# Kernel tuning notes

Measured on AMD Instinct MI355X. Metric: run time of the kernel, lower is better.

## Reference

```python
import jax, jax.numpy as jnp
import numpy as np

SA_LAMBDA = 1.0
IC_LAMBDA = 1.0
EPS = 1e-12  # torch F.normalize eps


def setup_inputs() -> dict:
    key = jax.random.key(0)
    k1, k2, k3, k4 = jax.random.split(key, 4)
    TF = jax.random.normal(k1, (16, 512, 32, 32), dtype=jnp.float32)
    SF = jax.random.normal(k2, (16, 512, 32, 32), dtype=jnp.float32)
    t_out = jax.random.normal(k3, (16, 21, 128, 128), dtype=jnp.float32)
    s_out = jax.random.normal(k4, (16, 21, 128, 128), dtype=jnp.float32)
    return {"TF": TF, "SF": SF, "t_out": t_out, "s_out": s_out}


def _l2_normalize_last(A):
    # matches torch.nn.functional.normalize(x, dim=2): x / max(||x||, eps)
    n = jnp.linalg.norm(A, axis=-1, keepdims=True)
    return A / jnp.maximum(n, EPS)


def _channel_weighted_spatial_gram(F4):
    # Algebraic fusion of einsum('bij,bki->bijk') + einsum('bijk,bi->bjk'):
    # ATT[b,m,n] = sum_c F[b,c,m] * F[b,c,n] * Fc[b,c]
    b, c, h, w = F4.shape
    Fc = jnp.sum(jnp.abs(F4), axis=(2, 3))          # [b, c]
    Fm = F4.reshape(b, c, h * w)                     # [b, c, M]
    A = jnp.einsum('bcm,bc,bcn->bmn', Fm, Fc, Fm)    # [b, M, M]
    return _l2_normalize_last(A)


def _normalized_channel_gram(L):
    # ICC[b,i,j] = sum_m L[b,i,m] * L[b,j,m], then L2-normalize along last dim
    G = jnp.einsum('bim,bjm->bij', L, L)
    return _l2_normalize_last(G)


def reference(TF, SF, t_out, s_out):
    b, c, h, w = TF.shape
    M = h * w
    ATT_T = _channel_weighted_spatial_gram(TF)
    ATT_S = _channel_weighted_spatial_gram(SF)
    diff = ATT_S - ATT_T
    SA_loss = SA_LAMBDA * jnp.sum(diff * diff) / (b * M ** 2)

    bb, cc, hh, ww = s_out.shape
    s_logit = s_out.reshape(bb, cc, hh * ww)
    t_logit = t_out.reshape(bb, cc, hh * ww)
    G_diff = _normalized_channel_gram(s_logit) - _normalized_channel_gram(t_logit)
    ic_loss = IC_LAMBDA * jnp.sum(G_diff * G_diff) / (cc * bb)

    return (s_out, ic_loss, SA_loss)
```

## Files before the change

kernel.cpp:

```cpp
#include <hip/hip_runtime.h>
#include <hip/hip_bf16.h>
#include <cstdint>
#include <cstddef>

typedef __bf16 bf16x8 __attribute__((ext_vector_type(8)));
typedef float f32x4 __attribute__((ext_vector_type(4)));

__device__ __forceinline__ void gload_lds16(const void* g, void* l) {
  __builtin_amdgcn_global_load_lds((const __attribute__((address_space(1))) void*)g,
                                   (__attribute__((address_space(3))) void*)l, 16, 0, 0);
}
__device__ __forceinline__ unsigned short f2bf(float x) {
  return __builtin_bit_cast(unsigned short, __float2bfloat16(x));
}
#define S_BARRIER asm volatile("s_barrier" ::: "memory")
#define WAIT_VM(N) asm volatile("s_waitcnt vmcnt(" #N ")" ::: "memory")

__global__ void fc_kernel(const float* __restrict__ TF, const float* __restrict__ SF,
                          float* __restrict__ sqrtFc) {
  int wv = threadIdx.x >> 6, lane = threadIdx.x & 63;
  int row = blockIdx.x * 4 + wv;
  const float* X = (row < 8192) ? TF : SF;
  const float* p = X + (size_t)(row & 8191) * 1024;
  float s = 0.f;
#pragma unroll
  for (int it = 0; it < 4; ++it) {
    float4 v = *reinterpret_cast<const float4*>(p + (size_t)(it * 64 + lane) * 4);
    s += fabsf(v.x) + fabsf(v.y) + fabsf(v.z) + fabsf(v.w);
  }
#pragma unroll
  for (int m = 32; m; m >>= 1) s += __shfl_xor(s, m);
  if (lane == 0) sqrtFc[row] = sqrtf(s);
}

__global__ void __launch_bounds__(256) wprep2_kernel(const float* __restrict__ TF,
                                                     const float* __restrict__ SF,
                                                     const float* __restrict__ sqrtFc,
                                                     __hip_bfloat16* __restrict__ Wt,
                                                     __hip_bfloat16* __restrict__ Ws) {
  __shared__ float lds[64][65];
  __shared__ float scale[64];
  int z = blockIdx.z;
  int t = z >> 4, b = z & 15;
  int m0 = blockIdx.x * 64, c0 = blockIdx.y * 64;
  const float* Xg = (t ? SF : TF) + (size_t)b * 524288;
  __hip_bfloat16* Wg = (t ? Ws : Wt) + (size_t)b * 524288;
  int tid = threadIdx.x;
  if (tid < 64) scale[tid] = sqrtFc[t * 8192 + b * 512 + c0 + tid];
#pragma unroll
  for (int i = 0; i < 4; ++i) {
    int v = i * 256 + tid;
    int r = v >> 4, q = v & 15;
    *reinterpret_cast<float4*>(&lds[r][q * 4]) =
        *reinterpret_cast<const float4*>(Xg + (size_t)(c0 + r) * 1024 + m0 + q * 4);
  }
  __syncthreads();
#pragma unroll
  for (int jj = 0; jj < 2; ++jj) {
    int m = jj * 32 + (tid >> 3), oct = tid & 7;
    union { unsigned short h[8]; uint4 u; } pk;
#pragma unroll
    for (int k = 0; k < 8; ++k) {
      int c = oct * 8 + k;
      pk.h[k] = f2bf(lds[c][m] * scale[c]);
    }
    *reinterpret_cast<uint4*>(Wg + (size_t)(m0 + m) * 512 + c0 + oct * 8) = pk.u;
  }
}

__global__ void __launch_bounds__(512, 4) syrk_fused_kernel(
    const __hip_bfloat16* __restrict__ Wt, const __hip_bfloat16* __restrict__ Ws,
    float* __restrict__ nT, float* __restrict__ nS, float* __restrict__ cross) {
  __shared__ __hip_bfloat16 AL[2][128 * 64];
  __shared__ __hip_bfloat16 BL[2][128 * 64];
  int bid = blockIdx.x;
  int j = (bid & 7) * 72 + (bid >> 3);
  int b = j / 36, pair = j % 36;
  int bx = pair, tm = 0;
  while (bx >= 8 - tm) { bx -= 8 - tm; ++tm; }
  int tn = tm + bx;
  bool diag = (tm == tn);
  const __hip_bfloat16* WTb = Wt + (size_t)b * 524288;
  const __hip_bfloat16* WSb = Ws + (size_t)b * 524288;
  const __hip_bfloat16* ATp = WTb + (size_t)tm * 65536;
  const __hip_bfloat16* ASp = WSb + (size_t)tm * 65536;
  const __hip_bfloat16* BTp = WTb + (size_t)tn * 65536;
  const __hip_bfloat16* BSp = WSb + (size_t)tn * 65536;

  const int tid = threadIdx.x;
  const int lane = tid & 63, wv = tid >> 6;
  const int wr = wv >> 1, wc = wv & 1;
  const int g = lane >> 4, c0 = lane & 15, cx = c0 & 7;

  int offs[2], dst[2];
#pragma unroll
  for (int i = 0; i < 2; ++i) {
    int ci = i * 512 + tid;
    int row = ci >> 3, slot = ci & 7;
    offs[i] = row * 512 + (slot ^ (row & 7)) * 8;
    dst[i] = (i * 512 + wv * 64) * 8;
  }

  f32x4 accT[2][4], accS[2][4];
#pragma unroll
  for (int mi = 0; mi < 2; ++mi)
#pragma unroll
    for (int ni = 0; ni < 4; ++ni) {
      accT[mi][ni] = (f32x4){0.f, 0.f, 0.f, 0.f};
      accS[mi][ni] = (f32x4){0.f, 0.f, 0.f, 0.f};
    }

  auto stage = [&](int s, int buf) {
    int kt = (s & 7) * 64;
    const __hip_bfloat16* Ab = (s < 8) ? ATp : ASp;
    const __hip_bfloat16* Bb = (s < 8) ? BTp : BSp;
#pragma unroll
    for (int i = 0; i < 2; ++i) {
      gload_lds16(Ab + offs[i] + kt, &AL[buf][dst[i]]);
      gload_lds16(Bb + offs[i] + kt, &BL[buf][dst[i]]);
    }
  };

  stage(0, 0);
#pragma unroll
  for (int s = 0; s < 16; ++s) {
    int buf = s & 1;
    if (s < 15) {
      stage(s + 1, buf ^ 1);
      WAIT_VM(4);
    } else {
      WAIT_VM(0);
    }
    S_BARRIER;
    const __hip_bfloat16* Ab = AL[buf];
    const __hip_bfloat16* Bb = BL[buf];
#pragma unroll
    for (int kk = 0; kk < 2; ++kk) {
      int ck = ((kk * 4 + g) ^ cx) * 8;
      bf16x8 av[2], bv[4];
#pragma unroll
      for (int mi = 0; mi < 2; ++mi)
        av[mi] = *reinterpret_cast<const bf16x8*>(Ab + (wr * 32 + mi * 16 + c0) * 64 + ck);
#pragma unroll
      for (int ni = 0; ni < 4; ++ni)
        bv[ni] = *reinterpret_cast<const bf16x8*>(Bb + (wc * 64 + ni * 16 + c0) * 64 + ck);
      if (s < 8) {
#pragma unroll
        for (int mi = 0; mi < 2; ++mi)
#pragma unroll
          for (int ni = 0; ni < 4; ++ni)
            accT[mi][ni] = __builtin_amdgcn_mfma_f32_16x16x32_bf16(av[mi], bv[ni], accT[mi][ni], 0, 0, 0);
      } else {
#pragma unroll
        for (int mi = 0; mi < 2; ++mi)
#pragma unroll
          for (int ni = 0; ni < 4; ++ni)
            accS[mi][ni] = __builtin_amdgcn_mfma_f32_16x16x32_bf16(av[mi], bv[ni], accS[mi][ni], 0, 0, 0);
      }
    }
    if (s < 15) S_BARRIER;
  }

  float* pT = nT + (size_t)b * 1024;
  float* pS = nS + (size_t)b * 1024;
  float* pC = cross + (size_t)b * 1024;
#pragma unroll
  for (int mi = 0; mi < 2; ++mi)
#pragma unroll
    for (int r = 0; r < 4; ++r) {
      float sT = 0.f, sS = 0.f, sC = 0.f;
#pragma unroll
      for (int ni = 0; ni < 4; ++ni) {
        float tv = accT[mi][ni][r], sv = accS[mi][ni][r];
        sT += tv * tv; sS += sv * sv; sC += tv * sv;
      }
#pragma unroll
      for (int msk = 1; msk < 16; msk <<= 1) {
        sT += __shfl_xor(sT, msk); sS += __shfl_xor(sS, msk); sC += __shfl_xor(sC, msk);
      }
      if (c0 == 0) {
        int m = tm * 128 + wr * 32 + mi * 16 + g * 4 + r;
        atomicAdd(pT + m, sT); atomicAdd(pS + m, sS); atomicAdd(pC + m, sC);
      }
    }
  if (!diag) {
#pragma unroll
    for (int ni = 0; ni < 4; ++ni) {
      float sT = 0.f, sS = 0.f, sC = 0.f;
#pragma unroll
      for (int mi = 0; mi < 2; ++mi)
#pragma unroll
        for (int r = 0; r < 4; ++r) {
          float tv = accT[mi][ni][r], sv = accS[mi][ni][r];
          sT += tv * tv; sS += sv * sv; sC += tv * sv;
        }
      sT += __shfl_xor(sT, 16); sS += __shfl_xor(sS, 16); sC += __shfl_xor(sC, 16);
      sT += __shfl_xor(sT, 32); sS += __shfl_xor(sS, 32); sC += __shfl_xor(sC, 32);
      if (g == 0) {
        int n = tn * 128 + wc * 64 + ni * 16 + c0;
        atomicAdd(pT + n, sT); atomicAdd(pS + n, sS); atomicAdd(pC + n, sC);
      }
    }
  }
}

__global__ void __launch_bounds__(256) icgram3_kernel(const float* __restrict__ t_out,
                                                      const float* __restrict__ s_out,
                                                      float* __restrict__ G,
                                                      float* __restrict__ outcpy) {
  __shared__ float lds[21 * 516];
  int chunk = blockIdx.x;
  int z = blockIdx.y;
  int t = z >> 4, bb = z & 15;
  const float* L = (t ? s_out : t_out) + (size_t)bb * 344064 + (size_t)chunk * 512;
  float* O = outcpy + (size_t)bb * 344064 + (size_t)chunk * 512;
  int tid = threadIdx.x;
  for (int idx = tid; idx < 21 * 128; idx += 256) {
    int r = idx >> 7, c = idx & 127;
    float4 v = *reinterpret_cast<const float4*>(L + (size_t)r * 16384 + c * 4);
    if (t) *reinterpret_cast<float4*>(O + (size_t)r * 16384 + c * 4) = v;
    *reinterpret_cast<float4*>(&lds[r * 516 + c * 4]) = v;
  }
  __syncthreads();
  int wv = tid >> 6, lane = tid & 63;
  float* Gz = G + (size_t)z * 441;
  for (int sp = wv; sp < 66; sp += 4) {
    int pp = sp, gi = 0;
    while (pp >= 11 - gi) { pp -= 11 - gi; ++gi; }
    int gj = gi + pp;
    int i0 = 2 * gi, j0 = 2 * gj;
    bool i1v = (i0 + 1 < 21), j1v = (j0 + 1 < 21);
    const float4* Ri0 = reinterpret_cast<const float4*>(&lds[i0 * 516]);
    const float4* Ri1 = reinterpret_cast<const float4*>(&lds[(i1v ? i0 + 1 : i0) * 516]);
    const float4* Rj0 = reinterpret_cast<const float4*>(&lds[j0 * 516]);
    const float4* Rj1 = reinterpret_cast<const float4*>(&lds[(j1v ? j0 + 1 : j0) * 516]);
    float4 a00 = Ri0[lane], a01 = Ri0[lane + 64];
    float4 a10 = Ri1[lane], a11 = Ri1[lane + 64];
    float4 b00 = Rj0[lane], b01 = Rj0[lane + 64];
    float4 b10 = Rj1[lane], b11 = Rj1[lane + 64];
    float s00 = a00.x * b00.x + a00.y * b00.y + a00.z * b00.z + a00.w * b00.w
              + a01.x * b01.x + a01.y * b01.y + a01.z * b01.z + a01.w * b01.w;
    float s01 = a00.x * b10.x + a00.y * b10.y + a00.z * b10.z + a00.w * b10.w
              + a01.x * b11.x + a01.y * b11.y + a01.z * b11.z + a01.w * b11.w;
    float s10 = a10.x * b00.x + a10.y * b00.y + a10.z * b00.z + a10.w * b00.w
              + a11.x * b01.x + a11.y * b01.y + a11.z * b01.z + a11.w * b01.w;
    float s11 = a10.x * b10.x + a10.y * b10.y + a10.z * b10.z + a10.w * b10.w
              + a11.x * b11.x + a11.y * b11.y + a11.z * b11.z + a11.w * b11.w;
    s00 += __shfl_xor(s00, 1); s00 += __shfl_xor(s00, 2);
    s01 += __shfl_xor(s01, 1); s01 += __shfl_xor(s01, 2);
    s10 += __shfl_xor(s10, 1); s10 += __shfl_xor(s10, 2);
    s11 += __shfl_xor(s11, 1); s11 += __shfl_xor(s11, 2);
    int q = lane & 3;
    float sq = (q == 0) ? s00 : (q == 1) ? s01 : (q == 2) ? s10 : s11;
    sq += __shfl_xor(sq, 4); sq += __shfl_xor(sq, 8);
    sq += __shfl_xor(sq, 16); sq += __shfl_xor(sq, 32);
    if (lane < 4) {
      bool ok = (lane == 0) || (lane == 1 && j1v) ||
                (lane == 2 && i1v && gi != gj) || (lane == 3 && i1v && j1v);
      int ii = (lane >> 1) ? i0 + 1 : i0;
      int jj = (lane & 1) ? j0 + 1 : j0;
      if (ok) atomicAdd(&Gz[ii * 21 + jj], sq);
    }
  }
}

__global__ void finalize_kernel(const float* __restrict__ G, const float* __restrict__ nT,
                                const float* __restrict__ nS, const float* __restrict__ cross,
                                float* __restrict__ out2) {
  __shared__ float red[16];
  int tid = threadIdx.x;
  float sa = 0.f;
#pragma unroll
  for (int it = 0; it < 4; ++it) {
    int i4 = it * 1024 + tid;
    float4 a = reinterpret_cast<const float4*>(nT)[i4];
    float4 s4 = reinterpret_cast<const float4*>(nS)[i4];
    float4 c4 = reinterpret_cast<const float4*>(cross)[i4];
#pragma unroll
    for (int k = 0; k < 4; ++k) {
      float a1 = (&a.x)[k], s1 = (&s4.x)[k], c1 = (&c4.x)[k];
      float NT = fmaxf(sqrtf(a1), 1e-12f), NS = fmaxf(sqrtf(s1), 1e-12f);
      sa += a1 / (NT * NT) + s1 / (NS * NS) - 2.f * c1 / (NT * NS);
    }
  }
  float ic = 0.f;
  if (tid < 336) {
    int b = tid / 21, i = tid % 21;
    const float* gt = G + (size_t)b * 441;
    const float* gs = G + (size_t)(16 + b) * 441;
    float nt = 0.f, ns = 0.f;
    for (int j = 0; j < 21; ++j) {
      int idx2 = (i <= j) ? i * 21 + j : j * 21 + i;
      float vt = gt[idx2], vs = gs[idx2];
      nt += vt * vt; ns += vs * vs;
    }
    float rt = 1.f / fmaxf(sqrtf(nt), 1e-12f);
    float rs = 1.f / fmaxf(sqrtf(ns), 1e-12f);
    for (int j = 0; j < 21; ++j) {
      int idx2 = (i <= j) ? i * 21 + j : j * 21 + i;
      float d = gs[idx2] * rs - gt[idx2] * rt;
      ic += d * d;
    }
  }
  int lane = tid & 63, wv = tid >> 6;
#pragma unroll
  for (int m = 32; m; m >>= 1) { sa += __shfl_xor(sa, m); ic += __shfl_xor(ic, m); }
  if (lane == 0) red[wv] = sa;
  __syncthreads();
  if (tid == 0) { float s = 0.f; for (int w = 0; w < 16; ++w) s += red[w]; out2[1] = s * (1.0f / 16777216.0f); }
  __syncthreads();
  if (lane == 0) red[wv] = ic;
  __syncthreads();
  if (tid == 0) { float s = 0.f; for (int w = 0; w < 16; ++w) s += red[w]; out2[0] = s * (1.0f / 336.0f); }
}

extern "C" void kernel_launch(void* const* d_in, const int* in_sizes, int n_in,
                              void* d_out, int out_size, void* d_ws, size_t ws_size,
                              hipStream_t stream) {
  const float* TF = (const float*)d_in[0];
  const float* SF = (const float*)d_in[1];
  const float* t_out = (const float*)d_in[2];
  const float* s_out = (const float*)d_in[3];
  float* out = (float*)d_out;
  char* ws = (char*)d_ws;

  float* nT = (float*)(ws + 0);
  float* nS = (float*)(ws + 65536);
  float* cross = (float*)(ws + 131072);
  float* G = (float*)(ws + 196608);
  float* sqrtFc = (float*)(ws + 253184);
  __hip_bfloat16* Wt = (__hip_bfloat16*)(ws + 318720);
  __hip_bfloat16* Ws = (__hip_bfloat16*)(ws + 318720 + 16777216);

  (void)hipMemsetAsync(ws, 0, 253056, stream);

  fc_kernel<<<4096, 256, 0, stream>>>(TF, SF, sqrtFc);
  wprep2_kernel<<<dim3(16, 8, 32), 256, 0, stream>>>(TF, SF, sqrtFc, Wt, Ws);
  syrk_fused_kernel<<<576, 512, 0, stream>>>(Wt, Ws, nT, nS, cross);
  icgram3_kernel<<<dim3(32, 32), 256, 0, stream>>>(t_out, s_out, G, out);
  finalize_kernel<<<1, 1024, 0, stream>>>(G, nT, nS, cross, out + 5505024);
}
```

Measured before the change: 131.9 us.

## Split IC gram into finer chunks, reduce in LDS, copy output via memcpy

The channel-gram kernel now processes 256-column chunks with 512-thread blocks across a 64x32 grid, giving more parallelism and smaller LDS tiles. Partial Gram sums are accumulated in shared memory first and flushed to global memory once per block, which cuts contention on global atomics. The s_out passthrough copy moves out of the kernel into a device-to-device hipMemcpyAsync. In exchange there are twice as many global atomic flush rounds and an extra copy operation on the stream.

New measurement: 126.2 us. 1.05x faster.

```diff
diff --git a/kernel.cpp b/kernel.cpp
--- a/kernel.cpp
+++ b/kernel.cpp
@@ -204,48 +204,40 @@
   }
 }
 
-__global__ void __launch_bounds__(256) icgram3_kernel(const float* __restrict__ t_out,
+__global__ void __launch_bounds__(512) icgram4_kernel(const float* __restrict__ t_out,
                                                       const float* __restrict__ s_out,
-                                                      float* __restrict__ G,
-                                                      float* __restrict__ outcpy) {
-  __shared__ float lds[21 * 516];
+                                                      float* __restrict__ G) {
+  __shared__ float lds[21 * 260];
+  __shared__ float Gs[441];
   int chunk = blockIdx.x;
   int z = blockIdx.y;
   int t = z >> 4, bb = z & 15;
-  const float* L = (t ? s_out : t_out) + (size_t)bb * 344064 + (size_t)chunk * 512;
-  float* O = outcpy + (size_t)bb * 344064 + (size_t)chunk * 512;
+  const float* L = (t ? s_out : t_out) + (size_t)bb * 344064 + (size_t)chunk * 256;
   int tid = threadIdx.x;
-  for (int idx = tid; idx < 21 * 128; idx += 256) {
-    int r = idx >> 7, c = idx & 127;
-    float4 v = *reinterpret_cast<const float4*>(L + (size_t)r * 16384 + c * 4);
-    if (t) *reinterpret_cast<float4*>(O + (size_t)r * 16384 + c * 4) = v;
-    *reinterpret_cast<float4*>(&lds[r * 516 + c * 4]) = v;
+  for (int i = tid; i < 441; i += 512) Gs[i] = 0.f;
+  for (int idx = tid; idx < 21 * 64; idx += 512) {
+    int r = idx >> 6, c = idx & 63;
+    *reinterpret_cast<float4*>(&lds[r * 260 + c * 4]) =
+        *reinterpret_cast<const float4*>(L + (size_t)r * 16384 + c * 4);
   }
   __syncthreads();
   int wv = tid >> 6, lane = tid & 63;
-  float* Gz = G + (size_t)z * 441;
-  for (int sp = wv; sp < 66; sp += 4) {
+  for (int sp = wv; sp < 66; sp += 8) {
     int pp = sp, gi = 0;
     while (pp >= 11 - gi) { pp -= 11 - gi; ++gi; }
     int gj = gi + pp;
     int i0 = 2 * gi, j0 = 2 * gj;
     bool i1v = (i0 + 1 < 21), j1v = (j0 + 1 < 21);
-    const float4* Ri0 = reinterpret_cast<const float4*>(&lds[i0 * 516]);
-    const float4* Ri1 = reinterpret_cast<const float4*>(&lds[(i1v ? i0 + 1 : i0) * 516]);
-    const float4* Rj0 = reinterpret_cast<const float4*>(&lds[j0 * 516]);
-    const float4* Rj1 = reinterpret_cast<const float4*>(&lds[(j1v ? j0 + 1 : j0) * 516]);
-    float4 a00 = Ri0[lane], a01 = Ri0[lane + 64];
-    float4 a10 = Ri1[lane], a11 = Ri1[lane + 64];
-    float4 b00 = Rj0[lane], b01 = Rj0[lane + 64];
-    float4 b10 = Rj1[lane], b11 = Rj1[lane + 64];
-    float s00 = a00.x * b00.x + a00.y * b00.y + a00.z * b00.z + a00.w * b00.w
-              + a01.x * b01.x + a01.y * b01.y + a01.z * b01.z + a01.w * b01.w;
-    float s01 = a00.x * b10.x + a00.y * b10.y + a00.z * b10.z + a00.w * b10.w
-              + a01.x * b11.x + a01.y * b11.y + a01.z * b11.z + a01.w * b11.w;
-    float s10 = a10.x * b00.x + a10.y * b00.y + a10.z * b00.z + a10.w * b00.w
-              + a11.x * b01.x + a11.y * b01.y + a11.z * b01.z + a11.w * b01.w;
-    float s11 = a10.x * b10.x + a10.y * b10.y + a10.z * b10.z + a10.w * b10.w
-              + a11.x * b11.x + a11.y * b11.y + a11.z * b11.z + a11.w * b11.w;
+    const float4* Ri0 = reinterpret_cast<const float4*>(&lds[i0 * 260]);
+    const float4* Ri1 = reinterpret_cast<const float4*>(&lds[(i1v ? i0 + 1 : i0) * 260]);
+    const float4* Rj0 = reinterpret_cast<const float4*>(&lds[j0 * 260]);
+    const float4* Rj1 = reinterpret_cast<const float4*>(&lds[(j1v ? j0 + 1 : j0) * 260]);
+    float4 a0 = Ri0[lane], a1 = Ri1[lane];
+    float4 b0 = Rj0[lane], b1 = Rj1[lane];
+    float s00 = a0.x * b0.x + a0.y * b0.y + a0.z * b0.z + a0.w * b0.w;
+    float s01 = a0.x * b1.x + a0.y * b1.y + a0.z * b1.z + a0.w * b1.w;
+    float s10 = a1.x * b0.x + a1.y * b0.y + a1.z * b0.z + a1.w * b0.w;
+    float s11 = a1.x * b1.x + a1.y * b1.y + a1.z * b1.z + a1.w * b1.w;
     s00 += __shfl_xor(s00, 1); s00 += __shfl_xor(s00, 2);
     s01 += __shfl_xor(s01, 1); s01 += __shfl_xor(s01, 2);
     s10 += __shfl_xor(s10, 1); s10 += __shfl_xor(s10, 2);
@@ -259,8 +251,14 @@
                 (lane == 2 && i1v && gi != gj) || (lane == 3 && i1v && j1v);
       int ii = (lane >> 1) ? i0 + 1 : i0;
       int jj = (lane & 1) ? j0 + 1 : j0;
-      if (ok) atomicAdd(&Gz[ii * 21 + jj], sq);
-    }
+      if (ok) atomicAdd(&Gs[ii * 21 + jj], sq);
+    }
+  }
+  __syncthreads();
+  float* Gz = G + (size_t)z * 441;
+  for (int i = tid; i < 441; i += 512) {
+    float v = Gs[i];
+    if (v != 0.f) atomicAdd(&Gz[i], v);
   }
 }
 
@@ -333,10 +331,12 @@
   __hip_bfloat16* Ws = (__hip_bfloat16*)(ws + 318720 + 16777216);
 
   (void)hipMemsetAsync(ws, 0, 253056, stream);
+  (void)hipMemcpyAsync(d_out, (const void*)s_out, (size_t)5505024 * 4,
+                       hipMemcpyDeviceToDevice, stream);
 
   fc_kernel<<<4096, 256, 0, stream>>>(TF, SF, sqrtFc);
   wprep2_kernel<<<dim3(16, 8, 32), 256, 0, stream>>>(TF, SF, sqrtFc, Wt, Ws);
   syrk_fused_kernel<<<576, 512, 0, stream>>>(Wt, Ws, nT, nS, cross);
-  icgram3_kernel<<<dim3(32, 32), 256, 0, stream>>>(t_out, s_out, G, out);
+  icgram4_kernel<<<dim3(64, 32), 512, 0, stream>>>(t_out, s_out, G);
   finalize_kernel<<<1, 1024, 0, stream>>>(G, nT, nS, cross, out + 5505024);
 }
```
